# Kernel optimization log

Measured on AMD Instinct MI355X. Metric: run time of the kernel, lower is better.

The kernel has to match this reference:

```python
import jax, jax.numpy as jnp
import numpy as np

DIM = 64; HEADS = 4; HD = DIM // HEADS; TOPK = 40; RS = 2  # region_size = max(4//t_patch,1)
B = 16; T = 2048; NR = T // RS
EPS = 1e-5
SCALE = DIM ** -0.5  # qk_scale=None -> self.dim**-0.5 (as in source, NOT head_dim)


def conv1d(x, w, pad, groups=1):
    return jax.lax.conv_general_dilated(x, w, (1,), [(pad, pad)],
        dimension_numbers=('NCH', 'OIH', 'NCH'), feature_group_count=groups)


def bn(x, g, b):
    # eval-mode BatchNorm1d with fresh running stats (mean=0, var=1)
    s = g * np.float32(1.0 / np.sqrt(1.0 + EPS))
    return x * s[None, :, None] + b[None, :, None]


def _blocks(t):
    # (B, C, T) -> (B, H, NR, RS, HD)
    return t.reshape(B, HEADS, HD, NR, RS).transpose(0, 1, 3, 4, 2)


def forward(x, n1_g, n1_b, wq, bnq_g, bnq_b, wk, bnk_g, bnk_b, wv,
            lepe_w, lepe_b, out_w, out_b, n2_g, n2_b,
            fc1_w, bn1_g, bn1_b, fr, fi, frb, fib, fc2_w, bn2_g, bn2_b):
    # ---------- Time_bra: top-k region routing attention ----------
    xn = bn(x, n1_g, n1_b)
    q = bn(conv1d(xn, wq, 1), bnq_g, bnq_b)
    k = bn(conv1d(xn, wk, 1), bnk_g, bnk_b)
    v = conv1d(xn, wv, 0)
    # region pooling on detached q/k (avg_pool1d, T divisible by RS)
    qd = jax.lax.stop_gradient(q); kd = jax.lax.stop_gradient(k)
    q_r = qd.reshape(B, DIM, NR, RS).mean(-1)
    k_r = kd.reshape(B, DIM, NR, RS).mean(-1)
    a_r = jnp.einsum('bcr,bcs->brs', q_r, k_r)          # (B, NR, NR) region affinity
    idx = jax.lax.top_k(a_r, TOPK)[1]                   # (B, NR, TOPK), shared across heads
    qb = _blocks(q); kb = _blocks(k); vb = _blocks(v)   # (B, H, NR, RS, HD)
    ie = idx[:, None, :, :, None, None]                 # (B, 1, NR, TOPK, 1, 1)
    kg = jnp.take_along_axis(kb[:, :, None], ie, axis=3).reshape(B, HEADS, NR, TOPK * RS, HD)
    vg = jnp.take_along_axis(vb[:, :, None], ie, axis=3).reshape(B, HEADS, NR, TOPK * RS, HD)
    logits = jnp.einsum('bhrqd,bhrkd->bhrqk', qb, kg) * jnp.float32(SCALE)
    attn = jax.nn.softmax(logits, axis=-1)
    o = jnp.einsum('bhrqk,bhrkd->bhrqd', attn, vg)      # (B, H, NR, RS, HD)
    o = o.transpose(0, 1, 4, 2, 3).reshape(B, DIM, T)
    o = o + conv1d(v, lepe_w, 1, groups=DIM) + lepe_b[None, :, None]  # lepe (depthwise)
    o = conv1d(o, out_w, 0) + out_b[None, :, None]
    x = x + o
    # ---------- Frequencydomain_FFN ----------
    yn = bn(x, n2_g, n2_b)
    h = jax.nn.relu(bn(conv1d(yn, fc1_w, 0), bn1_g, bn1_b))  # (B, 2C, T)
    h = h.transpose(0, 2, 1)                                  # (B, T, 2C)
    f = jnp.fft.fft(h, axis=1, norm='ortho')
    # torch.einsum('bnc,cc->bnc', x, r) contracts with diag(r) (repeated index)
    xr = jax.nn.relu(jnp.einsum('bnc,cc->bnc', f.real, fr) - jnp.einsum('bnc,cc->bnc', f.imag, fi) + frb)
    xi = jax.nn.relu(jnp.einsum('bnc,cc->bnc', f.imag, fr) + jnp.einsum('bnc,cc->bnc', f.real, fi) + fib)
    h = jnp.fft.ifft(jax.lax.complex(xr, xi), axis=1, norm='ortho').real.astype(jnp.float32)
    h = bn(conv1d(h.transpose(0, 2, 1), fc2_w, 0), bn2_g, bn2_b)
    return x + h


def setup_inputs() -> dict:
    ks = jax.random.split(jax.random.key(0), 16)
    C = DIM; C2 = 2 * DIM
    g = lambda i, shape, s: (s * jax.random.normal(ks[i], shape)).astype(jnp.float32)
    return {
        'x': jax.random.normal(ks[0], (B, C, T), dtype=jnp.float32),
        'n1_g': jnp.ones((C,), jnp.float32), 'n1_b': jnp.zeros((C,), jnp.float32),
        'wq': g(1, (C, C, 3), 0.05), 'bnq_g': jnp.ones((C,), jnp.float32), 'bnq_b': jnp.zeros((C,), jnp.float32),
        'wk': g(2, (C, C, 3), 0.05), 'bnk_g': jnp.ones((C,), jnp.float32), 'bnk_b': jnp.zeros((C,), jnp.float32),
        'wv': g(3, (C, C, 1), 0.05),
        'lepe_w': g(4, (C, 1, 3), 0.1), 'lepe_b': jnp.zeros((C,), jnp.float32),
        'out_w': g(5, (C, C, 1), 0.05), 'out_b': jnp.zeros((C,), jnp.float32),
        'n2_g': jnp.ones((C,), jnp.float32), 'n2_b': jnp.zeros((C,), jnp.float32),
        'fc1_w': g(6, (C2, C, 1), 0.05), 'bn1_g': jnp.ones((C2,), jnp.float32), 'bn1_b': jnp.zeros((C2,), jnp.float32),
        'fr': g(7, (C2, C2), 0.02), 'fi': g(8, (C2, C2), 0.02),
        'frb': g(9, (C2,), 0.02), 'fib': g(10, (C2,), 0.02),
        'fc2_w': g(11, (C, C2, 1), 0.05), 'bn2_g': jnp.ones((C,), jnp.float32), 'bn2_b': jnp.zeros((C,), jnp.float32),
    }


def reference(x, n1_g, n1_b, wq, bnq_g, bnq_b, wk, bnk_g, bnk_b, wv,
              lepe_w, lepe_b, out_w, out_b, n2_g, n2_b,
              fc1_w, bn1_g, bn1_b, fr, fi, frb, fib, fc2_w, bn2_g, bn2_b):
    return forward(x, n1_g, n1_b, wq, bnq_g, bnq_b, wk, bnk_g, bnk_b, wv,
                   lepe_w, lepe_b, out_w, out_b, n2_g, n2_b,
                   fc1_w, bn1_g, bn1_b, fr, fi, frb, fib, fc2_w, bn2_g, bn2_b)
```

## Files before the change

### kernel.cpp

```cpp
#include <hip/hip_runtime.h>
#include <hip/hip_bf16.h>

#define T 2048
#define NR 1024
#define TOPK 40

static __device__ __forceinline__ float bnscale() { return 0.9999950000374997f; }

static __device__ __forceinline__ unsigned wave_umax64(unsigned x) {
  unsigned r = x, t;
  t = (unsigned)__builtin_amdgcn_update_dpp((int)r, (int)r, 0x111, 0xf, 0xf, false); r = r > t ? r : t;
  t = (unsigned)__builtin_amdgcn_update_dpp((int)r, (int)r, 0x112, 0xf, 0xf, false); r = r > t ? r : t;
  t = (unsigned)__builtin_amdgcn_update_dpp((int)r, (int)r, 0x114, 0xf, 0xf, false); r = r > t ? r : t;
  t = (unsigned)__builtin_amdgcn_update_dpp((int)r, (int)r, 0x118, 0xf, 0xf, false); r = r > t ? r : t;
  t = (unsigned)__builtin_amdgcn_update_dpp((int)r, (int)r, 0x142, 0xf, 0xf, false); r = r > t ? r : t;
  t = (unsigned)__builtin_amdgcn_update_dpp((int)r, (int)r, 0x143, 0xf, 0xf, false); r = r > t ? r : t;
  return (unsigned)__builtin_amdgcn_readlane((int)r, 63);
}

__global__ __launch_bounds__(256) void k_qkv(
    const float* __restrict__ x, const float* __restrict__ n1_g, const float* __restrict__ n1_b,
    const float* __restrict__ wq, const float* __restrict__ bnq_g, const float* __restrict__ bnq_b,
    const float* __restrict__ wk, const float* __restrict__ bnk_g, const float* __restrict__ bnk_b,
    const float* __restrict__ wv,
    float* __restrict__ q_t, float* __restrict__ k_t, float* __restrict__ v_t,
    float* __restrict__ q_rc, float* __restrict__ k_rc)
{
  const int b = blockIdx.y;
  const int tile = blockIdx.x >> 2;
  const int oc0 = (blockIdx.x & 3) * 16;
  const int t0 = tile * 64;
  const int r0 = tile * 32;
  const int tid = threadIdx.x;
  const float INVS = bnscale();

  __shared__ float xn[64][67];
  __shared__ float ot[16][67];

  for (int i = tid; i < 64 * 66; i += 256) {
    int c = i / 66, tt = i - c * 66;
    int t = t0 + tt - 1;
    float v = (t >= 0 && t < T) ? x[(size_t)(b * 64 + c) * T + t] : 0.f;
    xn[c][tt] = v * (n1_g[c] * INVS) + n1_b[c];
  }
  __syncthreads();

  const int w = tid >> 6, lane = tid & 63;
  const int ob = oc0 + __builtin_amdgcn_readfirstlane(w) * 4;

  float accq[4], acck[4], accv[4];
#pragma unroll
  for (int j = 0; j < 4; ++j) { accq[j] = 0.f; acck[j] = 0.f; accv[j] = 0.f; }

#pragma unroll 1
  for (int c0 = 0; c0 < 64; c0 += 4) {
    float xr[4][3];
#pragma unroll
    for (int cc = 0; cc < 4; ++cc) {
      xr[cc][0] = xn[c0 + cc][lane];
      xr[cc][1] = xn[c0 + cc][lane + 1];
      xr[cc][2] = xn[c0 + cc][lane + 2];
    }
#pragma unroll
    for (int o4 = 0; o4 < 4; ++o4) {
      int o = ob + o4;
      const float* wqo = wq + o * 192 + c0 * 3;
      const float* wko = wk + o * 192 + c0 * 3;
      const float* wvo = wv + o * 64 + c0;
      float aq = accq[o4], ak = acck[o4], av = accv[o4];
#pragma unroll
      for (int cc = 0; cc < 4; ++cc) {
        aq += xr[cc][0] * wqo[cc * 3 + 0] + xr[cc][1] * wqo[cc * 3 + 1] + xr[cc][2] * wqo[cc * 3 + 2];
        ak += xr[cc][0] * wko[cc * 3 + 0] + xr[cc][1] * wko[cc * 3 + 1] + xr[cc][2] * wko[cc * 3 + 2];
        av += xr[cc][1] * wvo[cc];
      }
      accq[o4] = aq; acck[o4] = ak; accv[o4] = av;
    }
  }

#pragma unroll
  for (int o4 = 0; o4 < 4; ++o4) {
    int o = ob + o4;
    ot[o - oc0][lane] = accq[o4] * (bnq_g[o] * INVS) + bnq_b[o];
  }
  __syncthreads();
  for (int i = tid; i < 1024; i += 256) {
    int cl = i & 15, tt = i >> 4;
    q_t[((size_t)(b * T + t0 + tt)) * 64 + oc0 + cl] = ot[cl][tt];
  }
  for (int i = tid; i < 512; i += 256) {
    int rr = i & 31, cl = i >> 5;
    q_rc[((size_t)(b * 64 + oc0 + cl)) * NR + r0 + rr] = 0.5f * (ot[cl][2 * rr] + ot[cl][2 * rr + 1]);
  }
  __syncthreads();

#pragma unroll
  for (int o4 = 0; o4 < 4; ++o4) {
    int o = ob + o4;
    ot[o - oc0][lane] = acck[o4] * (bnk_g[o] * INVS) + bnk_b[o];
  }
  __syncthreads();
  for (int i = tid; i < 1024; i += 256) {
    int cl = i & 15, tt = i >> 4;
    k_t[((size_t)(b * T + t0 + tt)) * 64 + oc0 + cl] = ot[cl][tt];
  }
  for (int i = tid; i < 512; i += 256) {
    int rr = i & 31, cl = i >> 5;
    k_rc[((size_t)(b * 64 + oc0 + cl)) * NR + r0 + rr] = 0.5f * (ot[cl][2 * rr] + ot[cl][2 * rr + 1]);
  }
  __syncthreads();

#pragma unroll
  for (int o4 = 0; o4 < 4; ++o4) {
    ot[ob + o4 - oc0][lane] = accv[o4];
  }
  __syncthreads();
  for (int i = tid; i < 1024; i += 256) {
    int cl = i & 15, tt = i >> 4;
    v_t[((size_t)(b * T + t0 + tt)) * 64 + oc0 + cl] = ot[cl][tt];
  }
}

__global__ __launch_bounds__(256) void k_scores(
    const float* __restrict__ q_rc, const float* __restrict__ k_rc, int* __restrict__ sel)
{
  const int b = blockIdx.y;
  const int r0 = blockIdx.x * 16;
  const int tid = threadIdx.x;
  const int w = tid >> 6, lane = tid & 63;

  __shared__ float qsT[16][68];

  for (int i = tid; i < 1024; i += 256) {
    int rr = i & 15, c = i >> 4;
    qsT[rr][c] = q_rc[((size_t)(b * 64 + c)) * NR + r0 + rr];
  }
  __syncthreads();

  const int row0 = w * 4;

  float4 acc[4][4];
#pragma unroll
  for (int r = 0; r < 4; ++r)
#pragma unroll
    for (int j = 0; j < 4; ++j) acc[r][j] = make_float4(0.f, 0.f, 0.f, 0.f);

  const float4* kp = (const float4*)(k_rc + ((size_t)b * 64) * NR);
#pragma unroll 1
  for (int c0 = 0; c0 < 64; c0 += 4) {
    float4 qv[4];
#pragma unroll
    for (int r = 0; r < 4; ++r) qv[r] = *(const float4*)&qsT[row0 + r][c0];
#pragma unroll
    for (int cc = 0; cc < 4; ++cc) {
      const float4* kr = kp + (size_t)(c0 + cc) * 256 + lane;
      float4 k0 = kr[0], k1 = kr[64], k2 = kr[128], k3 = kr[192];
      float qf[4] = { (&qv[0].x)[cc], (&qv[1].x)[cc], (&qv[2].x)[cc], (&qv[3].x)[cc] };
#pragma unroll
      for (int r = 0; r < 4; ++r) {
        float q = qf[r];
        acc[r][0].x += q * k0.x; acc[r][0].y += q * k0.y; acc[r][0].z += q * k0.z; acc[r][0].w += q * k0.w;
        acc[r][1].x += q * k1.x; acc[r][1].y += q * k1.y; acc[r][1].z += q * k1.z; acc[r][1].w += q * k1.w;
        acc[r][2].x += q * k2.x; acc[r][2].y += q * k2.y; acc[r][2].z += q * k2.z; acc[r][2].w += q * k2.w;
        acc[r][3].x += q * k3.x; acc[r][3].y += q * k3.y; acc[r][3].z += q * k3.z; acc[r][3].w += q * k3.w;
      }
    }
  }

  unsigned pk[4][16];
#pragma unroll
  for (int r = 0; r < 4; ++r) {
#pragma unroll
    for (int j = 0; j < 4; ++j) {
      const float* av = &acc[r][j].x;
#pragma unroll
      for (int s = 0; s < 4; ++s) {
        unsigned u = __float_as_uint(av[s]);
        u ^= (unsigned)((int)u >> 31) | 0x80000000u;
        int idx = 256 * j + 4 * lane + s;
        pk[r][4 * j + s] = (u & 0xFFFFFC00u) | (unsigned)(1023 - idx);
      }
    }
#pragma unroll
    for (int k = 2; k <= 16; k <<= 1) {
#pragma unroll
      for (int j = k >> 1; j > 0; j >>= 1) {
#pragma unroll
        for (int i = 0; i < 16; ++i) {
          int l = i ^ j;
          if (l > i) {
            unsigned hi = pk[r][i] > pk[r][l] ? pk[r][i] : pk[r][l];
            unsigned lo = pk[r][i] > pk[r][l] ? pk[r][l] : pk[r][i];
            bool dir = ((i & k) == 0);
            pk[r][i] = dir ? hi : lo;
            pk[r][l] = dir ? lo : hi;
          }
        }
      }
    }
  }

  int res[4] = {0, 0, 0, 0};
#pragma unroll 1
  for (int it = 0; it < TOPK; ++it) {
#pragma unroll
    for (int r = 0; r < 4; ++r) {
      unsigned bv = wave_umax64(pk[r][0]);
      if (lane == it) res[r] = 1023 - (int)(bv & 1023u);
      bool won = (pk[r][0] == bv);
#pragma unroll
      for (int s = 0; s < 15; ++s) pk[r][s] = won ? pk[r][s + 1] : pk[r][s];
      pk[r][15] = won ? 0u : pk[r][15];
    }
  }

  if (lane < TOPK) {
#pragma unroll
    for (int r = 0; r < 4; ++r)
      sel[((size_t)(b * NR + r0 + row0 + r)) * TOPK + lane] = res[r];
  }
}

__global__ __launch_bounds__(256) void k_attn(
    const float* __restrict__ q_t, const float* __restrict__ k_t, const float* __restrict__ v_t,
    const int* __restrict__ sel, const float* __restrict__ lepe_w, const float* __restrict__ lepe_b,
    float* __restrict__ o_t)
{
  const int b = blockIdx.y;
  const int r = blockIdx.x;
  const int tid = threadIdx.x;

  __shared__ __align__(16) float kg[80][68];
  __shared__ __align__(16) float qb[2][64];
  __shared__ int   toff[80];
  __shared__ __align__(16) float lg[4][2][84];
  __shared__ float vl[4][64];

  float (*part)[2][64] = (float (*)[2][64])&kg[0][0];

  if (tid < 40) {
    int s = sel[((size_t)(b * NR + r)) * TOPK + tid];
    toff[2 * tid]     = s * 512;
    toff[2 * tid + 1] = s * 512 + 256;
  }
  if (tid >= 128 && tid < 256) {
    int i = tid - 128;
    int s = i >> 6, c = i & 63;
    qb[s][c] = q_t[((size_t)(b * T + r * 2 + s)) * 64 + c];
  }
  {
    int idx = tid >> 6, c = tid & 63;
    int t = 2 * r - 1 + idx;
    vl[idx][c] = (t >= 0 && t < T) ? v_t[((size_t)(b * T + t)) * 64 + c] : 0.f;
  }
  __syncthreads();

  {
    const char* kbase = (const char*)(k_t + (size_t)b * T * 64);
    for (int i = tid; i < 80 * 16; i += 256) {
      int row = i >> 4, c4 = i & 15;
      float4 kv = *(const float4*)(kbase + toff[row] + c4 * 16);
      *(float4*)&kg[row][c4 * 4] = kv;
    }
  }
  __syncthreads();

  const int h = tid >> 6, lane = tid & 63;

  {
    float4 q0[4], q1[4];
#pragma unroll
    for (int j = 0; j < 4; ++j) {
      q0[j] = *(const float4*)&qb[0][h * 16 + j * 4];
      q1[j] = *(const float4*)&qb[1][h * 16 + j * 4];
    }
    for (int col = lane; col < 80; col += 64) {
      float a0 = 0.f, a1 = 0.f;
#pragma unroll
      for (int j = 0; j < 4; ++j) {
        float4 kv = *(const float4*)&kg[col][h * 16 + j * 4];
        a0 += q0[j].x * kv.x + q0[j].y * kv.y + q0[j].z * kv.z + q0[j].w * kv.w;
        a1 += q1[j].x * kv.x + q1[j].y * kv.y + q1[j].z * kv.z + q1[j].w * kv.w;
      }
      lg[h][0][col] = a0 * 0.125f;
      lg[h][1][col] = a1 * 0.125f;
    }
  }

  for (int sq = 0; sq < 2; ++sq) {
    float a = lg[h][sq][lane];
    float bb = (lane < 16) ? lg[h][sq][64 + lane] : -INFINITY;
    float m = fmaxf(a, bb);
    for (int mm = 32; mm >= 1; mm >>= 1) m = fmaxf(m, __shfl_xor(m, mm));
    float ea = expf(a - m);
    float eb = (lane < 16) ? expf(bb - m) : 0.f;
    float ssum = ea + eb;
    for (int mm = 32; mm >= 1; mm >>= 1) ssum += __shfl_xor(ssum, mm);
    float inv = 1.f / ssum;
    lg[h][sq][lane] = ea * inv;
    if (lane < 16) lg[h][sq][64 + lane] = eb * inv;
  }
  __syncthreads();

  {
    const int c = tid & 63, j = tid >> 6;
    const int sq = j & 1, half = j >> 1;
    const int hh = c >> 4;
    const char* vbase = (const char*)(v_t + (size_t)b * T * 64) + c * 4;
    float acc = 0.f;
#pragma unroll 2
    for (int ch = 0; ch < 10; ++ch) {
      int col0 = half * 40 + ch * 4;
      float4 p = *(const float4*)&lg[hh][sq][col0];
      float v0 = *(const float*)(vbase + toff[col0 + 0]);
      float v1 = *(const float*)(vbase + toff[col0 + 1]);
      float v2 = *(const float*)(vbase + toff[col0 + 2]);
      float v3 = *(const float*)(vbase + toff[col0 + 3]);
      acc += p.x * v0 + p.y * v1 + p.z * v2 + p.w * v3;
    }
    part[half][sq][c] = acc;
  }
  __syncthreads();

  if (tid < 128) {
    int sq = tid >> 6, c = tid & 63;
    float o = part[0][sq][c] + part[1][sq][c];
    float lep = lepe_b[c];
#pragma unroll
    for (int kk = 0; kk < 3; ++kk) lep += lepe_w[c * 3 + kk] * vl[sq + kk][c];
    o_t[((size_t)(b * T + 2 * r + sq)) * 64 + c] = o + lep;
  }
}

__global__ __launch_bounds__(256) void k_mix(
    const float* __restrict__ x, const float* __restrict__ o_t,
    const float* __restrict__ out_w, const float* __restrict__ out_b,
    const float* __restrict__ n2_g, const float* __restrict__ n2_b,
    const float* __restrict__ fc1_w, const float* __restrict__ bn1_g, const float* __restrict__ bn1_b,
    float* __restrict__ xres, float* __restrict__ h_c)
{
  const int b = blockIdx.y;
  const int t0 = blockIdx.x * 16;
  const int tid = threadIdx.x;
  const float INVS = bnscale();

  __shared__ float ol[16][65];
  __shared__ float yn[16][65];
  __shared__ float xl[16][65];
  __shared__ float wo[64][65];
  __shared__ float w1[128][65];
  __shared__ float res2[128][17];

  for (int i = tid; i < 1024; i += 256) {
    int tt = i >> 6, c = i & 63;
    ol[tt][c] = o_t[((size_t)(b * T + t0 + tt)) * 64 + c];
  }
  for (int i = tid; i < 1024; i += 256) {
    int c = i >> 4, tt = i & 15;
    xl[tt][c] = x[(size_t)(b * 64 + c) * T + t0 + tt];
  }
  for (int i = tid; i < 4096; i += 256) {
    int c = i >> 6, cc = i & 63;
    wo[cc][c] = out_w[i];
  }
  for (int i = tid; i < 8192; i += 256) {
    int cc = i >> 6, c = i & 63;
    w1[cc][c] = fc1_w[i];
  }
  __syncthreads();

  {
    const int c = tid & 63, grp = tid >> 6;
    float a0 = out_b[c], a1 = a0, a2 = a0, a3 = a0;
    for (int cc = 0; cc < 64; ++cc) {
      float wv = wo[cc][c];
      a0 += wv * ol[grp * 4 + 0][cc];
      a1 += wv * ol[grp * 4 + 1][cc];
      a2 += wv * ol[grp * 4 + 2][cc];
      a3 += wv * ol[grp * 4 + 3][cc];
    }
    float g2 = n2_g[c] * INVS, b2 = n2_b[c];
    float av[4] = {a0, a1, a2, a3};
#pragma unroll
    for (int j = 0; j < 4; ++j) {
      int tt = grp * 4 + j;
      float xr = xl[tt][c] + av[j];
      xres[((size_t)(b * T + t0 + tt)) * 64 + c] = xr;
      yn[tt][c] = xr * g2 + b2;
    }
  }
  __syncthreads();

  {
    const int cc = tid & 127, half = tid >> 7;
    float acc[8];
#pragma unroll
    for (int j = 0; j < 8; ++j) acc[j] = 0.f;
    for (int c = 0; c < 64; ++c) {
      float wv = w1[cc][c];
#pragma unroll
      for (int j = 0; j < 8; ++j) acc[j] += wv * yn[half * 8 + j][c];
    }
    float g1 = bn1_g[cc] * INVS, b1 = bn1_b[cc];
#pragma unroll
    for (int j = 0; j < 8; ++j)
      res2[cc][half * 8 + j] = fmaxf(acc[j] * g1 + b1, 0.f);
  }
  __syncthreads();

  for (int i = tid; i < 2048; i += 256) {
    int tt = i & 15, cc = i >> 4;
    h_c[((size_t)(b * 128 + cc)) * T + t0 + tt] = res2[cc][tt];
  }
}

__global__ __launch_bounds__(256) void k_fft(
    const float* __restrict__ h_c, const float* __restrict__ fr, const float* __restrict__ fi,
    const float* __restrict__ frb, const float* __restrict__ fib, float* __restrict__ g_c)
{
  const int b = blockIdx.y;
  const int c2 = blockIdx.x;
  const int tid = threadIdx.x;

  __shared__ float re[2048];
  __shared__ float im[2048];
  __shared__ float twr[1024];
  __shared__ float twi[1024];

  for (int i = tid; i < 1024; i += 256) {
    float ang = -6.283185307179586f * (float)i * (1.0f / 2048.0f);
    float sn, cs;
    sincosf(ang, &sn, &cs);
    twr[i] = cs; twi[i] = sn;
  }
  const float* hrow = h_c + ((size_t)(b * 128 + c2)) * T;
  for (int t = tid; t < 2048; t += 256) {
    re[t] = hrow[t];
    im[t] = 0.f;
  }
  __syncthreads();

  for (int s = 11; s >= 1; --s) {
    const int half = 1 << (s - 1);
    for (int k = tid; k < 1024; k += 256) {
      int pos = k & (half - 1);
      int grp = k >> (s - 1);
      int i0 = (grp << s) + pos;
      int i1 = i0 + half;
      int j = pos << (11 - s);
      float wr = twr[j], wi = twi[j];
      float ur = re[i0], ui = im[i0];
      float vr = re[i1], vi = im[i1];
      re[i0] = ur + vr; im[i0] = ui + vi;
      float dr = ur - vr, di = ui - vi;
      re[i1] = dr * wr - di * wi;
      im[i1] = dr * wi + di * wr;
    }
    __syncthreads();
  }

  const float SC = 0.022097086912079608f;
  const float fa = fr[c2 * 129];
  const float fb = fi[c2 * 129];
  const float fra = frb[c2];
  const float fia = fib[c2];
  for (int t = tid; t < 2048; t += 256) {
    float rr = re[t] * SC, ii = im[t] * SC;
    re[t] = fmaxf(rr * fa - ii * fb + fra, 0.f);
    im[t] = fmaxf(ii * fa + rr * fb + fia, 0.f);
  }
  __syncthreads();

  for (int s = 1; s <= 11; ++s) {
    const int half = 1 << (s - 1);
    for (int k = tid; k < 1024; k += 256) {
      int pos = k & (half - 1);
      int grp = k >> (s - 1);
      int i0 = (grp << s) + pos;
      int i1 = i0 + half;
      int j = pos << (11 - s);
      float wr = twr[j], wi = -twi[j];
      float xr = re[i1], xi = im[i1];
      float tr = xr * wr - xi * wi;
      float ti = xr * wi + xi * wr;
      float ur = re[i0], ui = im[i0];
      re[i0] = ur + tr; im[i0] = ui + ti;
      re[i1] = ur - tr; im[i1] = ui - ti;
    }
    __syncthreads();
  }

  float* grow = g_c + ((size_t)(b * 128 + c2)) * T;
  for (int t = tid; t < 2048; t += 256)
    grow[t] = re[t] * SC;
}

__global__ __launch_bounds__(256) void k_out(
    const float* __restrict__ g_c, const float* __restrict__ xres,
    const float* __restrict__ fc2_w, const float* __restrict__ bn2_g, const float* __restrict__ bn2_b,
    float* __restrict__ out)
{
  const int b = blockIdx.y;
  const int t0 = blockIdx.x * 16;
  const int tid = threadIdx.x;
  const float INVS = bnscale();

  __shared__ float gl[16][129];
  __shared__ float w2[128][65];
  __shared__ float res[64][17];

  for (int i = tid; i < 2048; i += 256) {
    int tt = i & 15, cc = i >> 4;
    gl[tt][cc] = g_c[((size_t)(b * 128 + cc)) * T + t0 + tt];
  }
  for (int i = tid; i < 8192; i += 256) {
    int c = i >> 7, cc = i & 127;
    w2[cc][c] = fc2_w[i];
  }
  __syncthreads();

  {
    const int c = tid & 63, grp = tid >> 6;
    float a0 = 0.f, a1 = 0.f, a2 = 0.f, a3 = 0.f;
    for (int cc = 0; cc < 128; ++cc) {
      float wv = w2[cc][c];
      a0 += wv * gl[grp * 4 + 0][cc];
      a1 += wv * gl[grp * 4 + 1][cc];
      a2 += wv * gl[grp * 4 + 2][cc];
      a3 += wv * gl[grp * 4 + 3][cc];
    }
    float g2 = bn2_g[c] * INVS, b2 = bn2_b[c];
    float av[4] = {a0, a1, a2, a3};
#pragma unroll
    for (int j = 0; j < 4; ++j) {
      int tt = grp * 4 + j;
      res[c][tt] = xres[((size_t)(b * T + t0 + tt)) * 64 + c] + av[j] * g2 + b2;
    }
  }
  __syncthreads();

  for (int i = tid; i < 1024; i += 256) {
    int tt = i & 15, c = i >> 4;
    out[(size_t)(b * 64 + c) * T + t0 + tt] = res[c][tt];
  }
}

extern "C" void kernel_launch(void* const* d_in, const int* in_sizes, int n_in,
                              void* d_out, int out_size, void* d_ws, size_t ws_size,
                              hipStream_t stream) {
  (void)in_sizes; (void)n_in; (void)out_size; (void)ws_size;
  const float* x     = (const float*)d_in[0];
  const float* n1_g  = (const float*)d_in[1];
  const float* n1_b  = (const float*)d_in[2];
  const float* wq    = (const float*)d_in[3];
  const float* bnq_g = (const float*)d_in[4];
  const float* bnq_b = (const float*)d_in[5];
  const float* wk    = (const float*)d_in[6];
  const float* bnk_g = (const float*)d_in[7];
  const float* bnk_b = (const float*)d_in[8];
  const float* wv    = (const float*)d_in[9];
  const float* lepe_w= (const float*)d_in[10];
  const float* lepe_b= (const float*)d_in[11];
  const float* out_w = (const float*)d_in[12];
  const float* out_b = (const float*)d_in[13];
  const float* n2_g  = (const float*)d_in[14];
  const float* n2_b  = (const float*)d_in[15];
  const float* fc1_w = (const float*)d_in[16];
  const float* bn1_g = (const float*)d_in[17];
  const float* bn1_b = (const float*)d_in[18];
  const float* fr    = (const float*)d_in[19];
  const float* fi    = (const float*)d_in[20];
  const float* frb   = (const float*)d_in[21];
  const float* fib   = (const float*)d_in[22];
  const float* fc2_w = (const float*)d_in[23];
  const float* bn2_g = (const float*)d_in[24];
  const float* bn2_b = (const float*)d_in[25];

  float* out = (float*)d_out;
  float* ws  = (float*)d_ws;
  const size_t M1 = (size_t)1 << 20;

  float* q_t  = ws;
  float* k_t  = ws + 2 * M1;
  float* v_t  = ws + 4 * M1;
  float* q_rc = ws + 6 * M1;
  float* k_rc = ws + 7 * M1;
  float* o_t  = ws + 8 * M1;
  float* xrs  = ws + 10 * M1;
  int*   sel  = (int*)(ws + 12 * M1);
  float* h_c  = ws;
  float* g_c  = ws + 4 * M1;

  k_qkv<<<dim3(128, 16), 256, 0, stream>>>(x, n1_g, n1_b, wq, bnq_g, bnq_b,
                                           wk, bnk_g, bnk_b, wv, q_t, k_t, v_t, q_rc, k_rc);
  k_scores<<<dim3(64, 16), 256, 0, stream>>>(q_rc, k_rc, sel);
  k_attn<<<dim3(1024, 16), 256, 0, stream>>>(q_t, k_t, v_t, sel, lepe_w, lepe_b, o_t);
  k_mix<<<dim3(128, 16), 256, 0, stream>>>(x, o_t, out_w, out_b, n2_g, n2_b,
                                           fc1_w, bn1_g, bn1_b, xrs, h_c);
  k_fft<<<dim3(128, 16), 256, 0, stream>>>(h_c, fr, fi, frb, fib, g_c);
  k_out<<<dim3(128, 16), 256, 0, stream>>>(g_c, xrs, fc2_w, bn2_g, bn2_b, out);
}
```

Measured before the change: 457.4 us.

## Split top-k scoring across two key halves and merge candidates in attention

The region-scores kernel now launches twice as many blocks, each covering half of the 1024 key regions and emitting its own top-40 packed candidates with an 8-element bitonic sort instead of 16. The attention kernel loads both 40-candidate lists and merges them by rank counting in shared memory to build the gather offsets. This raises parallelism and lowers register pressure in the scoring kernel, at the cost of doubling the candidate output and adding a merge step plus a barrier to every attention block.

```diff
diff --git a/kernel.cpp b/kernel.cpp
--- a/kernel.cpp
+++ b/kernel.cpp
@@ -122,10 +122,11 @@
 }
 
 __global__ __launch_bounds__(256) void k_scores(
-    const float* __restrict__ q_rc, const float* __restrict__ k_rc, int* __restrict__ sel)
+    const float* __restrict__ q_rc, const float* __restrict__ k_rc, unsigned* __restrict__ cand)
 {
   const int b = blockIdx.y;
-  const int r0 = blockIdx.x * 16;
+  const int r0 = (blockIdx.x >> 1) * 16;
+  const int half = blockIdx.x & 1;
   const int tid = threadIdx.x;
   const int w = tid >> 6, lane = tid & 63;
 
@@ -139,13 +140,13 @@
 
   const int row0 = w * 4;
 
-  float4 acc[4][4];
+  float4 acc[4][2];
 #pragma unroll
   for (int r = 0; r < 4; ++r)
 #pragma unroll
-    for (int j = 0; j < 4; ++j) acc[r][j] = make_float4(0.f, 0.f, 0.f, 0.f);
-
-  const float4* kp = (const float4*)(k_rc + ((size_t)b * 64) * NR);
+    for (int j = 0; j < 2; ++j) acc[r][j] = make_float4(0.f, 0.f, 0.f, 0.f);
+
+  const float4* kp = (const float4*)(k_rc + ((size_t)b * 64) * NR) + half * 128;
 #pragma unroll 1
   for (int c0 = 0; c0 < 64; c0 += 4) {
     float4 qv[4];
@@ -154,39 +155,37 @@
 #pragma unroll
     for (int cc = 0; cc < 4; ++cc) {
       const float4* kr = kp + (size_t)(c0 + cc) * 256 + lane;
-      float4 k0 = kr[0], k1 = kr[64], k2 = kr[128], k3 = kr[192];
+      float4 k0 = kr[0], k1 = kr[64];
       float qf[4] = { (&qv[0].x)[cc], (&qv[1].x)[cc], (&qv[2].x)[cc], (&qv[3].x)[cc] };
 #pragma unroll
       for (int r = 0; r < 4; ++r) {
         float q = qf[r];
         acc[r][0].x += q * k0.x; acc[r][0].y += q * k0.y; acc[r][0].z += q * k0.z; acc[r][0].w += q * k0.w;
         acc[r][1].x += q * k1.x; acc[r][1].y += q * k1.y; acc[r][1].z += q * k1.z; acc[r][1].w += q * k1.w;
-        acc[r][2].x += q * k2.x; acc[r][2].y += q * k2.y; acc[r][2].z += q * k2.z; acc[r][2].w += q * k2.w;
-        acc[r][3].x += q * k3.x; acc[r][3].y += q * k3.y; acc[r][3].z += q * k3.z; acc[r][3].w += q * k3.w;
       }
     }
   }
 
-  unsigned pk[4][16];
+  unsigned pk[4][8];
 #pragma unroll
   for (int r = 0; r < 4; ++r) {
 #pragma unroll
-    for (int j = 0; j < 4; ++j) {
+    for (int j = 0; j < 2; ++j) {
       const float* av = &acc[r][j].x;
 #pragma unroll
       for (int s = 0; s < 4; ++s) {
         unsigned u = __float_as_uint(av[s]);
         u ^= (unsigned)((int)u >> 31) | 0x80000000u;
-        int idx = 256 * j + 4 * lane + s;
+        int idx = half * 512 + 256 * j + 4 * lane + s;
         pk[r][4 * j + s] = (u & 0xFFFFFC00u) | (unsigned)(1023 - idx);
       }
     }
 #pragma unroll
-    for (int k = 2; k <= 16; k <<= 1) {
+    for (int k = 2; k <= 8; k <<= 1) {
 #pragma unroll
       for (int j = k >> 1; j > 0; j >>= 1) {
 #pragma unroll
-        for (int i = 0; i < 16; ++i) {
+        for (int i = 0; i < 8; ++i) {
           int l = i ^ j;
           if (l > i) {
             unsigned hi = pk[r][i] > pk[r][l] ? pk[r][i] : pk[r][l];
@@ -200,30 +199,30 @@
     }
   }
 
-  int res[4] = {0, 0, 0, 0};
+  unsigned res[4] = {0u, 0u, 0u, 0u};
 #pragma unroll 1
   for (int it = 0; it < TOPK; ++it) {
 #pragma unroll
     for (int r = 0; r < 4; ++r) {
       unsigned bv = wave_umax64(pk[r][0]);
-      if (lane == it) res[r] = 1023 - (int)(bv & 1023u);
+      if (lane == it) res[r] = bv;
       bool won = (pk[r][0] == bv);
 #pragma unroll
-      for (int s = 0; s < 15; ++s) pk[r][s] = won ? pk[r][s + 1] : pk[r][s];
-      pk[r][15] = won ? 0u : pk[r][15];
+      for (int s = 0; s < 7; ++s) pk[r][s] = won ? pk[r][s + 1] : pk[r][s];
+      pk[r][7] = won ? 0u : pk[r][7];
     }
   }
 
   if (lane < TOPK) {
 #pragma unroll
     for (int r = 0; r < 4; ++r)
-      sel[((size_t)(b * NR + r0 + row0 + r)) * TOPK + lane] = res[r];
+      cand[(((size_t)(b * NR + r0 + row0 + r)) * 2 + half) * TOPK + lane] = res[r];
   }
 }
 
 __global__ __launch_bounds__(256) void k_attn(
     const float* __restrict__ q_t, const float* __restrict__ k_t, const float* __restrict__ v_t,
-    const int* __restrict__ sel, const float* __restrict__ lepe_w, const float* __restrict__ lepe_b,
+    const unsigned* __restrict__ cand, const float* __restrict__ lepe_w, const float* __restrict__ lepe_b,
     float* __restrict__ o_t)
 {
   const int b = blockIdx.y;
@@ -232,17 +231,14 @@
 
   __shared__ __align__(16) float kg[80][68];
   __shared__ __align__(16) float qb[2][64];
+  __shared__ unsigned cnd[80];
   __shared__ int   toff[80];
   __shared__ __align__(16) float lg[4][2][84];
   __shared__ float vl[4][64];
 
   float (*part)[2][64] = (float (*)[2][64])&kg[0][0];
 
-  if (tid < 40) {
-    int s = sel[((size_t)(b * NR + r)) * TOPK + tid];
-    toff[2 * tid]     = s * 512;
-    toff[2 * tid + 1] = s * 512 + 256;
-  }
+  if (tid < 80) cnd[tid] = cand[((size_t)(b * NR + r)) * 80 + tid];
   if (tid >= 128 && tid < 256) {
     int i = tid - 128;
     int s = i >> 6, c = i & 63;
@@ -252,6 +248,21 @@
     int idx = tid >> 6, c = tid & 63;
     int t = 2 * r - 1 + idx;
     vl[idx][c] = (t >= 0 && t < T) ? v_t[((size_t)(b * T + t)) * 64 + c] : 0.f;
+  }
+  __syncthreads();
+
+  if (tid < 80) {
+    unsigned v = cnd[tid];
+    int pos = (tid < 40) ? tid : tid - 40;
+    int other = (tid < 40) ? 40 : 0;
+    int rank = pos;
+#pragma unroll
+    for (int j = 0; j < 40; ++j) rank += (cnd[other + j] > v) ? 1 : 0;
+    if (rank < TOPK) {
+      int s = 1023 - (int)(v & 1023u);
+      toff[2 * rank]     = s * 512;
+      toff[2 * rank + 1] = s * 512 + 256;
+    }
   }
   __syncthreads();
 
@@ -587,14 +598,14 @@
   float* k_rc = ws + 7 * M1;
   float* o_t  = ws + 8 * M1;
   float* xrs  = ws + 10 * M1;
-  int*   sel  = (int*)(ws + 12 * M1);
+  unsigned* cand = (unsigned*)(ws + 12 * M1);
   float* h_c  = ws;
   float* g_c  = ws + 4 * M1;
 
   k_qkv<<<dim3(128, 16), 256, 0, stream>>>(x, n1_g, n1_b, wq, bnq_g, bnq_b,
                                            wk, bnk_g, bnk_b, wv, q_t, k_t, v_t, q_rc, k_rc);
-  k_scores<<<dim3(64, 16), 256, 0, stream>>>(q_rc, k_rc, sel);
-  k_attn<<<dim3(1024, 16), 256, 0, stream>>>(q_t, k_t, v_t, sel, lepe_w, lepe_b, o_t);
+  k_scores<<<dim3(128, 16), 256, 0, stream>>>(q_rc, k_rc, cand);
+  k_attn<<<dim3(1024, 16), 256, 0, stream>>>(q_t, k_t, v_t, cand, lepe_w, lepe_b, o_t);
   k_mix<<<dim3(128, 16), 256, 0, stream>>>(x, o_t, out_w, out_b, n2_g, n2_b,
                                            fc1_w, bn1_g, bn1_b, xrs, h_c);
   k_fft<<<dim3(128, 16), 256, 0, stream>>>(h_c, fr, fi, frb, fib, g_c);
```

New measurement: 480.2 us. 5.0% more time.
